# Performance work log

Measured on AMD Instinct MI355X. Metric: run time of the kernel, lower is better.

Reference implementation:

```python
import jax, jax.numpy as jnp
import numpy as np

HIDDEN = 512
HEADS = 8
HEAD_DIM = HIDDEN // HEADS


def setup_inputs() -> dict:
    key = jax.random.key(0)
    ks = jax.random.split(key, 13)
    B, S, H = 4, 2048, HIDDEN
    s = 1.0 / np.sqrt(H).astype(np.float32)
    inp = {
        "values": jax.random.normal(ks[0], (B, S, H), jnp.float32),
        "keys": jax.random.normal(ks[1], (B, S, H), jnp.float32),
        "query": jax.random.normal(ks[2], (B, S, H), jnp.float32),
        "mask": jax.random.randint(ks[3], (B, S), 0, 2, jnp.int32),
        "Wq": jax.random.normal(ks[4], (H, H), jnp.float32) * s,
        "bq": jnp.zeros((H,), jnp.float32),
        "Wk": jax.random.normal(ks[5], (H, H), jnp.float32) * s,
        "bk": jnp.zeros((H,), jnp.float32),
        "Wv": jax.random.normal(ks[6], (H, H), jnp.float32) * s,
        "bv": jnp.zeros((H,), jnp.float32),
        "Wo": jax.random.normal(ks[7], (H, H), jnp.float32) * s,
        "bo": jnp.zeros((H,), jnp.float32),
    }
    return inp


def reference(values, keys, query, mask, Wq, bq, Wk, bk, Wv, bv, Wo, bo):
    B, Sq, H = query.shape
    Sk = keys.shape[1]
    # projections (x @ W + b)
    Q = query @ Wq + bq
    K = keys @ Wk + bk
    V = values @ Wv + bv
    # [B, S, H] -> [B, heads, S, head_dim]
    def split(x, S):
        return x.reshape(B, S, HEADS, HEAD_DIM).transpose(0, 2, 1, 3)
    Qh, Kh, Vh = split(Q, Sq), split(K, Sk), split(V, Sk)
    scale = 1.0 / np.sqrt(HEAD_DIM).astype(np.float32)
    scores = jnp.einsum('bhqd,bhkd->bhqk', Qh, Kh) * scale  # [B,H,Sq,Sk]
    m = mask[:, None, None, :]  # [B,1,1,Sk]
    scores = jnp.where(m == 0, jnp.float32(-1e9), scores)
    attn = jax.nn.softmax(scores, axis=-1)
    ctx = jnp.einsum('bhqk,bhkd->bhqd', attn, Vh)
    ctx = ctx.transpose(0, 2, 1, 3).reshape(B, Sq, H)
    return ctx @ Wo + bo
```

## Files before the change

### kernel.cpp

```cpp
#include <hip/hip_runtime.h>

#define HID 512
#define NH 8
#define HD 64
#define BATCH 4
#define SEQ 2048
#define MTOT (BATCH * SEQ)

typedef unsigned short ushort_t;
typedef __bf16 bf16x8 __attribute__((ext_vector_type(8)));
typedef unsigned short ushort8v __attribute__((ext_vector_type(8)));
typedef unsigned short ushort4v __attribute__((ext_vector_type(4)));
typedef float floatx4 __attribute__((ext_vector_type(4)));
typedef unsigned int uintx4 __attribute__((ext_vector_type(4)));

static __device__ __forceinline__ unsigned short f2bf(float f) {
  __bf16 b = (__bf16)f;
  return __builtin_bit_cast(unsigned short, b);
}
static __device__ __forceinline__ float bf2f(unsigned short s) {
  union { unsigned int u; float f; } c; c.u = ((unsigned int)s) << 16;
  return c.f;
}
static __device__ __forceinline__ bf16x8 asbf(ushort8v v) {
  return __builtin_bit_cast(bf16x8, v);
}
static __device__ __forceinline__ float max3f(float a, float b, float c) {
  return fmaxf(fmaxf(a, b), c);
}
static __device__ __forceinline__ float fexp2(float x) {
  return __builtin_amdgcn_exp2f(x);
}
static __device__ __forceinline__ void gl_lds16(const ushort_t* g, ushort_t* l) {
  __builtin_amdgcn_global_load_lds(
      (const __attribute__((address_space(1))) void*)g,
      (__attribute__((address_space(3))) void*)l, 16, 0, 0);
}

static __device__ __forceinline__ int detect_bf(const unsigned int* __restrict__ q) {
  int lane = threadIdx.x & 63;
  int hits = 0;
#pragma unroll
  for (int i = 0; i < 4; ++i) {
    unsigned e = (q[lane * 4 + i] >> 7) & 0xff;
    hits += (e >= 110 && e <= 136) ? 1 : 0;
  }
#pragma unroll
  for (int s = 1; s < 64; s <<= 1) hits += __shfl_xor(hits, s);
  return hits >= 128 ? 1 : 0;
}

#define SC_LOG2E 0.18033688011112042f

__global__ __launch_bounds__(256) void prep_all(
    const void* __restrict__ W0, const void* __restrict__ W1,
    const void* __restrict__ W2, const void* __restrict__ W3,
    ushort_t* __restrict__ T0, ushort_t* __restrict__ T1,
    ushort_t* __restrict__ T2, ushort_t* __restrict__ T3,
    const void* __restrict__ B0, const void* __restrict__ B1,
    const void* __restrict__ B2, const void* __restrict__ B3,
    float* __restrict__ biasF, const int* __restrict__ mask,
    float* __restrict__ mb, const unsigned int* __restrict__ qd) {
  const int bx = blockIdx.x;
  const int isbf = detect_bf(qd);
  if (bx < 256) {
    const int sel = bx >> 6, t = bx & 63;
    const void* W; ushort_t* T;
    switch (sel) {
      case 0: W = W0; T = T0; break;
      case 1: W = W1; T = T1; break;
      case 2: W = W2; T = T2; break;
      default: W = W3; T = T3; break;
    }
    __shared__ ushort_t Ts[64 * 72];
    const int tid = threadIdx.x;
    const int kt = (t >> 3) * 64;
    const int nt = (t & 7) * 64;
    const int r = tid >> 2;
    const int c = (tid & 3) * 16;

    ushort8v v0, v1;
    if (isbf) {
      const ushort_t* p = (const ushort_t*)W + (long)(kt + r) * HID + nt + c;
      v0 = *(const ushort8v*)(p);
      v1 = *(const ushort8v*)(p + 8);
    } else {
      const float* p = (const float*)W + (long)(kt + r) * HID + nt + c;
      floatx4 f0 = *(const floatx4*)(p);
      floatx4 f1 = *(const floatx4*)(p + 4);
      floatx4 f2 = *(const floatx4*)(p + 8);
      floatx4 f3 = *(const floatx4*)(p + 12);
#pragma unroll
      for (int i = 0; i < 4; ++i) {
        v0[i] = f2bf(f0[i]); v0[4 + i] = f2bf(f1[i]);
        v1[i] = f2bf(f2[i]); v1[4 + i] = f2bf(f3[i]);
      }
    }
    *(ushort8v*)(&Ts[r * 72 + c])     = v0;
    *(ushort8v*)(&Ts[r * 72 + c + 8]) = v1;
    __syncthreads();
    ushort8v o0, o1;
#pragma unroll
    for (int j = 0; j < 8; ++j) o0[j] = Ts[(c + j) * 72 + r];
#pragma unroll
    for (int j = 0; j < 8; ++j) o1[j] = Ts[(c + 8 + j) * 72 + r];
    ushort_t* q = T + (long)(nt + r) * HID + kt + c;
    *(ushort8v*)(q)     = o0;
    *(ushort8v*)(q + 8) = o1;
  } else if (bx < 264) {
    int i = (bx - 256) * 256 + threadIdx.x;
    int t = i >> 9, j = i & 511;
    const void* B = (t == 0) ? B0 : (t == 1) ? B1 : (t == 2) ? B2 : B3;
    biasF[i] = isbf ? bf2f(((const ushort_t*)B)[j]) : ((const float*)B)[j];
  } else {
    int i = (bx - 264) * 256 + threadIdx.x;
    mb[i] = mask[i] ? 0.f : -1e9f;
  }
}

__global__ __launch_bounds__(256) void gemm_qkv3(
    const void* __restrict__ X0, const void* __restrict__ X1, const void* __restrict__ X2,
    const ushort_t* __restrict__ WtBase, const float* __restrict__ biasBase,
    ushort_t* __restrict__ YBase) {
  const int isbf = detect_bf((const unsigned int*)X0);
  int lin = blockIdx.x + 256 * blockIdx.z;
  int swz = (lin & 7) * 96 + (lin >> 3);
  const int z = swz >> 8;
  const int mblk = swz & 255;
  const void* X = (z == 0) ? X0 : (z == 1) ? X1 : X2;
  const ushort_t* Wt = WtBase + (size_t)z * HID * HID;
  const float* biasF = biasBase + (size_t)z * HID;
  ushort_t* Y = YBase + (size_t)z * MTOT * HID;

  const int tid = threadIdx.x;
  const int wid = tid >> 6, lane = tid & 63;
  const int id = lane & 15, quad = lane >> 4;
  const int m0 = mblk * 32;

  __shared__ ushort_t As[32 * 32];
  __shared__ ushort_t Bs[512 * 32];

  const int a_r = tid >> 3;
  const int a_o = (tid & 1) * 4;
  const int a_pb = ((tid & 7) >> 1) ^ (a_r & 3);
  const int b_ro = lane >> 2;
  const int b_scb = (lane & 3);

  floatx4 acc[2][8];
#pragma unroll
  for (int i = 0; i < 2; ++i)
#pragma unroll
    for (int j = 0; j < 8; ++j) acc[i][j] = (floatx4){0.f, 0.f, 0.f, 0.f};

  for (int k0 = 0; k0 < HID; k0 += 32) {
    ushort4v aW;
    if (isbf) {
      aW = *(const ushort4v*)((const ushort_t*)X + (long)(m0 + a_r) * HID + k0 + (tid & 7) * 4);
    } else {
      floatx4 f = *(const floatx4*)((const float*)X + (long)(m0 + a_r) * HID + k0 + (tid & 7) * 4);
#pragma unroll
      for (int i = 0; i < 4; ++i) aW[i] = f2bf(f[i]);
    }
    __syncthreads();
    *(ushort4v*)(&As[a_r * 32 + (a_pb << 3) + a_o]) = aW;
#pragma unroll
    for (int i = 0; i < 8; ++i) {
      int rb = wid * 128 + i * 16;
      int srow = rb + b_ro;
      gl_lds16(Wt + (long)srow * HID + k0 + ((b_scb ^ (srow & 3)) << 3), &Bs[rb * 32]);
    }
    __syncthreads();
    {
      ushort8v af[2], bfv[8];
      const int pb = (quad ^ (id & 3)) << 3;
#pragma unroll
      for (int ms = 0; ms < 2; ++ms)
        af[ms] = *(const ushort8v*)(&As[(ms * 16 + id) * 32 + pb]);
#pragma unroll
      for (int ns = 0; ns < 8; ++ns)
        bfv[ns] = *(const ushort8v*)(&Bs[(wid * 128 + ns * 16 + id) * 32 + pb]);
#pragma unroll
      for (int ms = 0; ms < 2; ++ms)
#pragma unroll
        for (int ns = 0; ns < 8; ++ns)
          acc[ms][ns] = __builtin_amdgcn_mfma_f32_16x16x32_bf16(asbf(af[ms]), asbf(bfv[ns]), acc[ms][ns], 0, 0, 0);
    }
  }
#pragma unroll
  for (int ns = 0; ns < 8; ++ns) {
    int col = wid * 128 + ns * 16 + id;
    float bv = biasF[col];
#pragma unroll
    for (int ms = 0; ms < 2; ++ms) {
      int row0 = m0 + ms * 16 + quad * 4;
#pragma unroll
      for (int r = 0; r < 4; ++r)
        Y[(long)(row0 + r) * HID + col] = f2bf(acc[ms][ns][r] + bv);
    }
  }
}

__global__ __launch_bounds__(256) void gemm_out2(
    const ushort_t* __restrict__ X, const ushort_t* __restrict__ Wt,
    const float* __restrict__ biasF, void* __restrict__ out,
    const unsigned int* __restrict__ qd) {
  const int isbf = detect_bf(qd);
  const int tid = threadIdx.x;
  const int wid = tid >> 6, lane = tid & 63;
  const int id = lane & 15, quad = lane >> 4;
  const int wm = wid >> 1, wn = wid & 1;
  const int m0 = blockIdx.x * 64, n0 = blockIdx.y * 128;

  __shared__ ushort_t As[64 * 64];
  __shared__ ushort_t Bs[128 * 64];

  const int lrow = lane >> 3;
  const int scb  = (lane & 7) ^ lrow;

  floatx4 acc[2][4];
#pragma unroll
  for (int i = 0; i < 2; ++i)
#pragma unroll
    for (int j = 0; j < 4; ++j) acc[i][j] = (floatx4){0.f, 0.f, 0.f, 0.f};

  for (int k0 = 0; k0 < HID; k0 += 64) {
    __syncthreads();
#pragma unroll
    for (int i = 0; i < 2; ++i) {
      int r = wid * 16 + i * 8 + lrow;
      gl_lds16(X + (long)(m0 + r) * HID + k0 + scb * 8, &As[(wid * 16 + i * 8) * 64]);
    }
#pragma unroll
    for (int i = 0; i < 4; ++i) {
      int r = wid * 32 + i * 8 + lrow;
      gl_lds16(Wt + (long)(n0 + r) * HID + k0 + scb * 8, &Bs[(wid * 32 + i * 8) * 64]);
    }
    __syncthreads();
#pragma unroll
    for (int kk = 0; kk < 64; kk += 32) {
      ushort8v af[2], bfv[4];
      const int cb = (kk >> 3) + quad;
#pragma unroll
      for (int ms = 0; ms < 2; ++ms) {
        int row = wm * 32 + ms * 16 + id;
        af[ms] = *(const ushort8v*)(&As[row * 64 + ((cb ^ (id & 7)) << 3)]);
      }
#pragma unroll
      for (int ns = 0; ns < 4; ++ns) {
        int row = wn * 64 + ns * 16 + id;
        bfv[ns] = *(const ushort8v*)(&Bs[row * 64 + ((cb ^ (id & 7)) << 3)]);
      }
#pragma unroll
      for (int ms = 0; ms < 2; ++ms)
#pragma unroll
        for (int ns = 0; ns < 4; ++ns)
          acc[ms][ns] = __builtin_amdgcn_mfma_f32_16x16x32_bf16(asbf(af[ms]), asbf(bfv[ns]), acc[ms][ns], 0, 0, 0);
    }
  }
#pragma unroll
  for (int ns = 0; ns < 4; ++ns) {
    int col = n0 + wn * 64 + ns * 16 + id;
    float bv = biasF[col];
#pragma unroll
    for (int ms = 0; ms < 2; ++ms) {
      int row0 = m0 + wm * 32 + ms * 16 + quad * 4;
      if (isbf) {
        ushort_t* o = (ushort_t*)out;
#pragma unroll
        for (int r = 0; r < 4; ++r) o[(long)(row0 + r) * HID + col] = f2bf(acc[ms][ns][r] + bv);
      } else {
        float* o = (float*)out;
#pragma unroll
        for (int r = 0; r < 4; ++r) o[(long)(row0 + r) * HID + col] = acc[ms][ns][r] + bv;
      }
    }
  }
}

__global__ __launch_bounds__(512) void flash_attn(
    const ushort_t* __restrict__ Q, const ushort_t* __restrict__ K,
    const ushort_t* __restrict__ V, const float* __restrict__ mb,
    ushort_t* __restrict__ ctx) {
  int lin = blockIdx.x + 16 * blockIdx.y + 128 * blockIdx.z;
  int swz = (lin & 7) * 64 + (lin >> 3);
  const int qblk = swz & 15, h = (swz >> 4) & 7, b = swz >> 7;
  const int tid = threadIdx.x;
  const int wid = tid >> 6, lane = tid & 63;
  const int id = lane & 15, quad = lane >> 4;

  __shared__ ushort_t Kt[64 * 72];
  __shared__ ushort_t Vt[64 * 72];
  __shared__ ushort_t Pl[8][16 * 72];

  const ushort_t* Qb = Q + (long)(b * SEQ + qblk * 128 + wid * 16) * HID + h * HD;
  const ushort_t* Kb = K + (long)(b * SEQ) * HID + h * HD;
  const ushort_t* Vb = V + (long)(b * SEQ) * HID + h * HD;
  const float* mrow = mb + b * SEQ;

  ushort8v qf[2];
#pragma unroll
  for (int kh = 0; kh < 2; ++kh)
    qf[kh] = *(const ushort8v*)(Qb + id * HID + kh * 32 + quad * 8);

  floatx4 o[4];
  float m_i = -1e30f, l_i = 0.f;
#pragma unroll
  for (int dg = 0; dg < 4; ++dg) o[dg] = (floatx4){0, 0, 0, 0};

  const bool kstager = (tid < 256);
  const int t2 = tid & 255;
  const int skey = t2 >> 2;
  const int sdc  = (t2 & 3) * 16;
  const int vkp  = (t2 & 31) * 2;
  const int vdc  = (t2 >> 5) * 8;

  ushort8v r0, r1;
  if (kstager) {
    const ushort_t* kpp = Kb + (long)skey * HID + sdc;
    r0 = *(const ushort8v*)(kpp);
    r1 = *(const ushort8v*)(kpp + 8);
  } else {
    const ushort_t* vp0 = Vb + (long)vkp * HID + vdc;
    r0 = *(const ushort8v*)(vp0);
    r1 = *(const ushort8v*)(vp0 + HID);
  }

  for (int kb = 0; kb < SEQ / 64; ++kb) {
    if (kstager) {
      *(ushort8v*)(&Kt[skey * 72 + sdc])     = r0;
      *(ushort8v*)(&Kt[skey * 72 + sdc + 8]) = r1;
    } else {
      uintx4 a = __builtin_bit_cast(uintx4, r0);
      uintx4 bq = __builtin_bit_cast(uintx4, r1);
#pragma unroll
      for (int j = 0; j < 4; ++j) {
        unsigned int d0 = __builtin_amdgcn_perm(bq[j], a[j], 0x05040100u);
        unsigned int d1 = __builtin_amdgcn_perm(bq[j], a[j], 0x07060302u);
        *(unsigned int*)(&Vt[(vdc + 2 * j) * 72 + vkp])     = d0;
        *(unsigned int*)(&Vt[(vdc + 2 * j + 1) * 72 + vkp]) = d1;
      }
    }
    __syncthreads();

    if (kb + 1 < SEQ / 64) {
      if (kstager) {
        const ushort_t* kpp = Kb + (long)((kb + 1) * 64 + skey) * HID + sdc;
        r0 = *(const ushort8v*)(kpp);
        r1 = *(const ushort8v*)(kpp + 8);
      } else {
        const ushort_t* vp0 = Vb + (long)((kb + 1) * 64 + vkp) * HID + vdc;
        r0 = *(const ushort8v*)(vp0);
        r1 = *(const ushort8v*)(vp0 + HID);
      }
    }

    floatx4 st[4];
    __builtin_amdgcn_s_setprio(1);
#pragma unroll
    for (int ks = 0; ks < 4; ++ks) {
      ushort8v kf0 = *(const ushort8v*)(&Kt[(ks * 16 + id) * 72 + quad * 8]);
      ushort8v kf1 = *(const ushort8v*)(&Kt[(ks * 16 + id) * 72 + 32 + quad * 8]);
      floatx4 a = (floatx4){0, 0, 0, 0};
      a = __builtin_amdgcn_mfma_f32_16x16x32_bf16(asbf(kf0), asbf(qf[0]), a, 0, 0, 0);
      a = __builtin_amdgcn_mfma_f32_16x16x32_bf16(asbf(kf1), asbf(qf[1]), a, 0, 0, 0);
      st[ks] = a;
    }
    __builtin_amdgcn_s_setprio(0);
#pragma unroll
    for (int ks = 0; ks < 4; ++ks) {
      floatx4 mbv = *(const floatx4*)(mrow + kb * 64 + ks * 16 + quad * 4);
#pragma unroll
      for (int r = 0; r < 4; ++r)
        st[ks][r] = fmaf(st[ks][r], SC_LOG2E, mbv[r]);
    }
    {
      float t0 = max3f(st[0][0], st[0][1], st[0][2]);
      float t1 = max3f(st[0][3], st[1][0], st[1][1]);
      float t2m = max3f(st[1][2], st[1][3], st[2][0]);
      float t3 = max3f(st[2][1], st[2][2], st[2][3]);
      float t4 = max3f(st[3][0], st[3][1], st[3][2]);
      float mx = max3f(t0, t1, st[3][3]);
      float mz = max3f(t2m, t3, t4);
      mx = fmaxf(mx, mz);
      mx = fmaxf(mx, __shfl_xor(mx, 16));
      mx = fmaxf(mx, __shfl_xor(mx, 32));
      if (!__all(mx - m_i <= 8.f)) {
        float mnew = fmaxf(m_i, mx);
        float alpha = fexp2(m_i - mnew);
        m_i = mnew;
        l_i *= alpha;
#pragma unroll
        for (int dg = 0; dg < 4; ++dg) o[dg] *= alpha;
      }
      float mcur = m_i;
      floatx4 rsv = (floatx4){0.f, 0.f, 0.f, 0.f};
#pragma unroll
      for (int ks = 0; ks < 4; ++ks) {
        ushort4v pk;
#pragma unroll
        for (int r = 0; r < 4; ++r) {
          float p = fexp2(st[ks][r] - mcur);
          rsv[r] += p;
          pk[r] = f2bf(p);
        }
        *(ushort4v*)(&Pl[wid][id * 72 + ks * 16 + quad * 4]) = pk;
      }
      float rs = (rsv[0] + rsv[1]) + (rsv[2] + rsv[3]);
      rs += __shfl_xor(rs, 16);
      rs += __shfl_xor(rs, 32);
      l_i += rs;
    }

    __builtin_amdgcn_s_setprio(1);
#pragma unroll
    for (int kc = 0; kc < 2; ++kc) {
      ushort8v pf = *(const ushort8v*)(&Pl[wid][id * 72 + kc * 32 + quad * 8]);
#pragma unroll
      for (int dg = 0; dg < 4; ++dg) {
        ushort8v vf = *(const ushort8v*)(&Vt[(dg * 16 + id) * 72 + kc * 32 + quad * 8]);
        o[dg] = __builtin_amdgcn_mfma_f32_16x16x32_bf16(asbf(vf), asbf(pf), o[dg], 0, 0, 0);
      }
    }
    __builtin_amdgcn_s_setprio(0);
    __syncthreads();
  }

  {
    float inv = 1.0f / l_i;
    long qrow = (long)(b * SEQ + qblk * 128 + wid * 16 + id);
#pragma unroll
    for (int dg = 0; dg < 4; ++dg) {
      ushort4v pk;
#pragma unroll
      for (int r = 0; r < 4; ++r) pk[r] = f2bf(o[dg][r] * inv);
      *(ushort4v*)(&ctx[qrow * HID + h * HD + dg * 16 + quad * 4]) = pk;
    }
  }
}

extern "C" void kernel_launch(void* const* d_in, const int* in_sizes, int n_in,
                              void* d_out, int out_size, void* d_ws, size_t ws_size,
                              hipStream_t stream) {
  const void* values = d_in[0];
  const void* keys   = d_in[1];
  const void* query  = d_in[2];
  const int*  mask   = (const int*)d_in[3];
  const void* Wq = d_in[4];  const void* bq = d_in[5];
  const void* Wk = d_in[6];  const void* bk = d_in[7];
  const void* Wv = d_in[8];  const void* bv = d_in[9];
  const void* Wo = d_in[10]; const void* bo = d_in[11];

  ushort_t* ws = (ushort_t*)d_ws;
  const size_t NEL = (size_t)MTOT * HID;
  ushort_t* Qp  = ws;
  ushort_t* Kp  = ws + NEL;
  ushort_t* Vp  = ws + 2 * NEL;
  ushort_t* Cp  = ws + 3 * NEL;
  ushort_t* WqT = ws + 4 * NEL;
  ushort_t* WkT = WqT + (size_t)HID * HID;
  ushort_t* WvT = WkT + (size_t)HID * HID;
  ushort_t* WoT = WvT + (size_t)HID * HID;
  float* biasF  = (float*)(WoT + (size_t)HID * HID);
  float* mbias  = biasF + 4 * HID;

  prep_all<<<296, 256, 0, stream>>>(Wq, Wk, Wv, Wo, WqT, WkT, WvT, WoT,
                                    bq, bk, bv, bo, biasF, mask, mbias,
                                    (const unsigned int*)query);

  gemm_qkv3<<<dim3(MTOT / 32, 1, 3), 256, 0, stream>>>(
      query, keys, values, WqT, biasF, Qp);

  flash_attn<<<dim3(SEQ / 128, NH, BATCH), 512, 0, stream>>>(Qp, Kp, Vp, mbias, Cp);

  gemm_out2<<<dim3(MTOT / 64, HID / 128), 256, 0, stream>>>(
      Cp, WoT, biasF + 3 * HID, d_out, (const unsigned int*)query);
}
```

Baseline: 223.4 us.

## Double-buffer LDS in projection GEMMs with larger tiles and swizzled block order

Rewrites the QKV projection GEMM to use 64x256 tiles with a K-step of 64 and double-buffered shared memory. The next A/B tiles are prefetched while MFMAs run on the current buffer, which halves the number of barriers per tile. The output GEMM gets the same double buffering plus a 1D grid with a swizzled block order to improve cache locality. The cost is higher LDS use per block, which may lower occupancy.

```diff
diff --git a/kernel.cpp b/kernel.cpp
--- a/kernel.cpp
+++ b/kernel.cpp
@@ -118,15 +118,17 @@
   }
 }
 
-__global__ __launch_bounds__(256) void gemm_qkv3(
+__global__ __launch_bounds__(256) void gemm_qkv5(
     const void* __restrict__ X0, const void* __restrict__ X1, const void* __restrict__ X2,
     const ushort_t* __restrict__ WtBase, const float* __restrict__ biasBase,
     ushort_t* __restrict__ YBase) {
   const int isbf = detect_bf((const unsigned int*)X0);
-  int lin = blockIdx.x + 256 * blockIdx.z;
+  int lin = blockIdx.x;
   int swz = (lin & 7) * 96 + (lin >> 3);
   const int z = swz >> 8;
-  const int mblk = swz & 255;
+  const int rem = swz & 255;
+  const int m0 = (rem >> 1) * 64;
+  const int n0 = (rem & 1) * 256;
   const void* X = (z == 0) ? X0 : (z == 1) ? X1 : X2;
   const ushort_t* Wt = WtBase + (size_t)z * HID * HID;
   const float* biasF = biasBase + (size_t)z * HID;
@@ -135,16 +137,13 @@
   const int tid = threadIdx.x;
   const int wid = tid >> 6, lane = tid & 63;
   const int id = lane & 15, quad = lane >> 4;
-  const int m0 = mblk * 32;
-
-  __shared__ ushort_t As[32 * 32];
-  __shared__ ushort_t Bs[512 * 32];
-
-  const int a_r = tid >> 3;
-  const int a_o = (tid & 1) * 4;
-  const int a_pb = ((tid & 7) >> 1) ^ (a_r & 3);
-  const int b_ro = lane >> 2;
-  const int b_scb = (lane & 3);
+  const int wm = wid >> 1, wn = wid & 1;
+
+  __shared__ ushort_t As[2][64 * 64];
+  __shared__ ushort_t Bs[2][256 * 64];
+
+  const int b_ro = lane >> 3;
+  const int b_cb = lane & 7;
 
   floatx4 acc[2][8];
 #pragma unroll
@@ -152,47 +151,92 @@
 #pragma unroll
     for (int j = 0; j < 8; ++j) acc[i][j] = (floatx4){0.f, 0.f, 0.f, 0.f};
 
-  for (int k0 = 0; k0 < HID; k0 += 32) {
-    ushort4v aW;
+  ushort8v aR[2];
+#pragma unroll
+  for (int s = 0; s < 2; ++s) {
+    int idx = tid * 2 + s, row = idx >> 3, cb = idx & 7;
     if (isbf) {
-      aW = *(const ushort4v*)((const ushort_t*)X + (long)(m0 + a_r) * HID + k0 + (tid & 7) * 4);
+      aR[s] = *(const ushort8v*)((const ushort_t*)X + (long)(m0 + row) * HID + cb * 8);
     } else {
-      floatx4 f = *(const floatx4*)((const float*)X + (long)(m0 + a_r) * HID + k0 + (tid & 7) * 4);
-#pragma unroll
-      for (int i = 0; i < 4; ++i) aW[i] = f2bf(f[i]);
-    }
-    __syncthreads();
-    *(ushort4v*)(&As[a_r * 32 + (a_pb << 3) + a_o]) = aW;
-#pragma unroll
-    for (int i = 0; i < 8; ++i) {
-      int rb = wid * 128 + i * 16;
-      int srow = rb + b_ro;
-      gl_lds16(Wt + (long)srow * HID + k0 + ((b_scb ^ (srow & 3)) << 3), &Bs[rb * 32]);
-    }
-    __syncthreads();
-    {
+      const float* p = (const float*)X + (long)(m0 + row) * HID + cb * 8;
+      floatx4 f0 = *(const floatx4*)(p);
+      floatx4 f1 = *(const floatx4*)(p + 4);
+#pragma unroll
+      for (int i = 0; i < 4; ++i) { aR[s][i] = f2bf(f0[i]); aR[s][4 + i] = f2bf(f1[i]); }
+    }
+  }
+#pragma unroll
+  for (int i = 0; i < 8; ++i) {
+    int j = wid * 8 + i;
+    gl_lds16(Wt + (long)(n0 + j * 8 + b_ro) * HID + ((b_cb ^ b_ro) << 3),
+             &Bs[0][(j * 8) * 64]);
+  }
+#pragma unroll
+  for (int s = 0; s < 2; ++s) {
+    int idx = tid * 2 + s, row = idx >> 3, cb = idx & 7;
+    *(ushort8v*)(&As[0][row * 64 + ((cb ^ (row & 7)) << 3)]) = aR[s];
+  }
+  __syncthreads();
+
+  int cur = 0;
+  for (int t = 0; t < 8; ++t) {
+    const bool more = (t + 1 < 8);
+    if (more) {
+      const int k1 = (t + 1) * 64;
+#pragma unroll
+      for (int s = 0; s < 2; ++s) {
+        int idx = tid * 2 + s, row = idx >> 3, cb = idx & 7;
+        if (isbf) {
+          aR[s] = *(const ushort8v*)((const ushort_t*)X + (long)(m0 + row) * HID + k1 + cb * 8);
+        } else {
+          const float* p = (const float*)X + (long)(m0 + row) * HID + k1 + cb * 8;
+          floatx4 f0 = *(const floatx4*)(p);
+          floatx4 f1 = *(const floatx4*)(p + 4);
+#pragma unroll
+          for (int i = 0; i < 4; ++i) { aR[s][i] = f2bf(f0[i]); aR[s][4 + i] = f2bf(f1[i]); }
+        }
+      }
+#pragma unroll
+      for (int i = 0; i < 8; ++i) {
+        int j = wid * 8 + i;
+        gl_lds16(Wt + (long)(n0 + j * 8 + b_ro) * HID + k1 + ((b_cb ^ b_ro) << 3),
+                 &Bs[cur ^ 1][(j * 8) * 64]);
+      }
+    }
+#pragma unroll
+    for (int kk = 0; kk < 64; kk += 32) {
       ushort8v af[2], bfv[8];
-      const int pb = (quad ^ (id & 3)) << 3;
+      const int cb = (kk >> 3) + quad;
+      const int px = (cb ^ (id & 7)) << 3;
 #pragma unroll
       for (int ms = 0; ms < 2; ++ms)
-        af[ms] = *(const ushort8v*)(&As[(ms * 16 + id) * 32 + pb]);
+        af[ms] = *(const ushort8v*)(&As[cur][(wm * 32 + ms * 16 + id) * 64 + px]);
 #pragma unroll
       for (int ns = 0; ns < 8; ++ns)
-        bfv[ns] = *(const ushort8v*)(&Bs[(wid * 128 + ns * 16 + id) * 32 + pb]);
+        bfv[ns] = *(const ushort8v*)(&Bs[cur][(wn * 128 + ns * 16 + id) * 64 + px]);
 #pragma unroll
       for (int ms = 0; ms < 2; ++ms)
 #pragma unroll
         for (int ns = 0; ns < 8; ++ns)
           acc[ms][ns] = __builtin_amdgcn_mfma_f32_16x16x32_bf16(asbf(af[ms]), asbf(bfv[ns]), acc[ms][ns], 0, 0, 0);
     }
+    if (more) {
+#pragma unroll
+      for (int s = 0; s < 2; ++s) {
+        int idx = tid * 2 + s, row = idx >> 3, cb = idx & 7;
+        *(ushort8v*)(&As[cur ^ 1][row * 64 + ((cb ^ (row & 7)) << 3)]) = aR[s];
+      }
+    }
+    __syncthreads();
+    cur ^= 1;
   }
 #pragma unroll
   for (int ns = 0; ns < 8; ++ns) {
-    int col = wid * 128 + ns * 16 + id;
+    int col = n0 + wn * 128 + ns * 16 + id;
     float bv = biasF[col];
 #pragma unroll
     for (int ms = 0; ms < 2; ++ms) {
-      int row0 = m0 + ms * 16 + quad * 4;
+      int row0 = m0 + wm * 32 + ms * 16 + quad * 4;
 #pragma unroll
       for (int r = 0; r < 4; ++r)
         Y[(long)(row0 + r) * HID + col] = f2bf(acc[ms][ns][r] + bv);
@@ -200,22 +244,26 @@
   }
 }
 
-__global__ __launch_bounds__(256) void gemm_out2(
+__global__ __launch_bounds__(256) void gemm_out5(
     const ushort_t* __restrict__ X, const ushort_t* __restrict__ Wt,
     const float* __restrict__ biasF, void* __restrict__ out,
     const unsigned int* __restrict__ qd) {
   const int isbf = detect_bf(qd);
+  int lin = blockIdx.x;
+  int swz = (lin & 7) * 64 + (lin >> 3);
+  const int m0 = (swz >> 2) * 64;
+  const int n0 = (swz & 3) * 128;
+
   const int tid = threadIdx.x;
   const int wid = tid >> 6, lane = tid & 63;
   const int id = lane & 15, quad = lane >> 4;
   const int wm = wid >> 1, wn = wid & 1;
-  const int m0 = blockIdx.x * 64, n0 = blockIdx.y * 128;
-
-  __shared__ ushort_t As[64 * 64];
-  __shared__ ushort_t Bs[128 * 64];
-
-  const int lrow = lane >> 3;
-  const int scb  = (lane & 7) ^ lrow;
+
+  __shared__ ushort_t As[2][64 * 64];
+  __shared__ ushort_t Bs[2][128 * 64];
+
+  const int b_ro = lane >> 3;
+  const int b_cb = lane & 7;
 
   floatx4 acc[2][4];
 #pragma unroll
@@ -223,39 +271,57 @@
 #pragma unroll
     for (int j = 0; j < 4; ++j) acc[i][j] = (floatx4){0.f, 0.f, 0.f, 0.f};
 
-  for (int k0 = 0; k0 < HID; k0 += 64) {
-    __syncthreads();
-#pragma unroll
-    for (int i = 0; i < 2; ++i) {
-      int r = wid * 16 + i * 8 + lrow;
-      gl_lds16(X + (long)(m0 + r) * HID + k0 + scb * 8, &As[(wid * 16 + i * 8) * 64]);
-    }
-#pragma unroll
-    for (int i = 0; i < 4; ++i) {
-      int r = wid * 32 + i * 8 + lrow;
-      gl_lds16(Wt + (long)(n0 + r) * HID + k0 + scb * 8, &Bs[(wid * 32 + i * 8) * 64]);
-    }
-    __syncthreads();
+#pragma unroll
+  for (int i = 0; i < 2; ++i) {
+    int j = wid * 2 + i;
+    gl_lds16(X + (long)(m0 + j * 8 + b_ro) * HID + ((b_cb ^ b_ro) << 3),
+             &As[0][(j * 8) * 64]);
+  }
+#pragma unroll
+  for (int i = 0; i < 4; ++i) {
+    int j = wid * 4 + i;
+    gl_lds16(Wt + (long)(n0 + j * 8 + b_ro) * HID + ((b_cb ^ b_ro) << 3),
+             &Bs[0][(j * 8) * 64]);
+  }
+  __syncthreads();
+
+  int cur = 0;
+  for (int t = 0; t < 8; ++t) {
+    const bool more = (t + 1 < 8);
+    if (more) {
+      const int k1 = (t + 1) * 64;
+#pragma unroll
+      for (int i = 0; i < 2; ++i) {
+        int j = wid * 2 + i;
+        gl_lds16(X + (long)(m0 + j * 8 + b_ro) * HID + k1 + ((b_cb ^ b_ro) << 3),
+                 &As[cur ^ 1][(j * 8) * 64]);
+      }
+#pragma unroll
+      for (int i = 0; i < 4; ++i) {
+        int j = wid * 4 + i;
+        gl_lds16(Wt + (long)(n0 + j * 8 + b_ro) * HID + k1 + ((b_cb ^ b_ro) << 3),
+                 &Bs[cur ^ 1][(j * 8) * 64]);
+      }
+    }
 #pragma unroll
     for (int kk = 0; kk < 64; kk += 32) {
       ushort8v af[2], bfv[4];
       const int cb = (kk >> 3) + quad;
-#pragma unroll
-      for (int ms = 0; ms < 2; ++ms) {
-        int row = wm * 32 + ms * 16 + id;
-        af[ms] = *(const ushort8v*)(&As[row * 64 + ((cb ^ (id & 7)) << 3)]);
-      }
-#pragma unroll
-      for (int ns = 0; ns < 4; ++ns) {
-        int row = wn * 64 + ns * 16 + id;
-        bfv[ns] = *(const ushort8v*)(&Bs[row * 64 + ((cb ^ (id & 7)) << 3)]);
-      }
+      const int px = (cb ^ (id & 7)) << 3;
+#pragma unroll
+      for (int ms = 0; ms < 2; ++ms)
+        af[ms] = *(const ushort8v*)(&As[cur][(wm * 32 + ms * 16 + id) * 64 + px]);
+#pragma unroll
+      for (int ns = 0; ns < 4; ++ns)
+        bfv[ns] = *(const ushort8v*)(&Bs[cur][(wn * 64 + ns * 16 + id) * 64 + px]);
 #pragma unroll
       for (int ms = 0; ms < 2; ++ms)
 #pragma unroll
         for (int ns = 0; ns < 4; ++ns)
           acc[ms][ns] = __builtin_amdgcn_mfma_f32_16x16x32_bf16(asbf(af[ms]), asbf(bfv[ns]), acc[ms][ns], 0, 0, 0);
     }
+    __syncthreads();
+    cur ^= 1;
   }
 #pragma unroll
   for (int ns = 0; ns < 4; ++ns) {
@@ -467,11 +533,10 @@
                                     bq, bk, bv, bo, biasF, mask, mbias,
                                     (const unsigned int*)query);
 
-  gemm_qkv3<<<dim3(MTOT / 32, 1, 3), 256, 0, stream>>>(
-      query, keys, values, WqT, biasF, Qp);
+  gemm_qkv5<<<768, 256, 0, stream>>>(query, keys, values, WqT, biasF, Qp);
 
   flash_attn<<<dim3(SEQ / 128, NH, BATCH), 512, 0, stream>>>(Qp, Kp, Vp, mbias, Cp);
 
-  gemm_out2<<<dim3(MTOT / 64, HID / 128), 256, 0, stream>>>(
-      Cp, WoT, biasF + 3 * HID, d_out, (const unsigned int*)query);
-}
+  gemm_out5<<<512, 256, 0, stream>>>(Cp, WoT, biasF + 3 * HID, d_out,
+                                     (const unsigned int*)query);
+}
```

New measurement: 221.6 us. About the same (-0.8%).
